# Performance work log

Measured on AMD Instinct MI355X. Metric: run time of the kernel, lower is better.

The kernel has to match this reference:

```python
import jax, jax.numpy as jnp
import numpy as np

N = 128                      # reduced state dimension (Q_dim[0])
S = N * (N + 1) // 2         # number of triu pairwise products = 8256
BATCH = 16384                # snapshot columns
_rows, _cols = np.triu_indices(N)
ROWS = jnp.asarray(_rows)    # [S] int32 constants
COLS = jnp.asarray(_cols)


def setup_inputs() -> dict:
    key = jax.random.key(0)
    kx, ka, kb = jax.random.split(key, 3)
    x = jax.random.normal(kx, (N, BATCH), dtype=jnp.float32)
    # learned operators (module inits them to zeros; use small random for a meaningful baseline)
    A = jax.random.normal(ka, (N, N), dtype=jnp.float32) * 0.02
    B = jax.random.normal(kb, (N, S), dtype=jnp.float32) * 0.02
    return {"x": x, "A": A, "B": B}


def reference(x, A, B):
    # quadratic feature expansion: x2[k, :] = x[i_k, :] * x[j_k, :] over triu pairs
    x2 = x[ROWS] * x[COLS]                 # [S, BATCH]
    return A @ x + B @ x2                  # [N, BATCH]
```

## Files before the change

### kernel.cpp

```cpp
#include <hip/hip_runtime.h>


constexpr int N_     = 128;
constexpr int S_     = 8256;
constexpr int BATCH_ = 16384;
constexpr int KTOT   = 8384;
constexpr int NKT    = 131;
constexpr size_t WT_BYTES = (size_t)KTOT * 128 * 2;
constexpr size_t PP_OFF   = WT_BYTES;
constexpr size_t XH_OFF   = PP_OFF + 32768;

typedef __attribute__((ext_vector_type(8))) _Float16 half8;
typedef __attribute__((ext_vector_type(2))) _Float16 half2t;
typedef __attribute__((ext_vector_type(4))) float f32x4;

typedef __attribute__((address_space(1))) const unsigned int gas_u32;
typedef __attribute__((address_space(3))) unsigned int las_u32;

__device__ __forceinline__ ushort f2h(float f) {
    _Float16 h = (_Float16)f;
    ushort b; __builtin_memcpy(&b, &h, 2); return b;
}
__device__ __forceinline__ float h2f(ushort b) {
    _Float16 h; __builtin_memcpy(&h, &b, 2); return (float)h;
}
__device__ __forceinline__ half2t duph(ushort b) {
    uint w = ((uint)b << 16) | (uint)b;
    half2t d; __builtin_memcpy(&d, &w, 4); return d;
}
__device__ __forceinline__ half8 mul_bc(half8 w, half2t d) {
    union { half8 h; half2t p[4]; } u, r;
    u.h = w;
    #pragma unroll
    for (int q = 0; q < 4; ++q) r.p[q] = u.p[q] * d;
    return r.h;
}

__device__ __forceinline__ int cumN(int i) {
    if (i <= 0) return 0;
    const int n = i - 1, t = n >> 3, r = n & 7;
    return 16 * i - (4 * t * (t + 1) + r * (t + 1));
}
__device__ __forceinline__ int offR(int i) {
    const int a = i >> 3, b = i & 7;
    const int p = b ? (8 * (b - 1) - (((b - 1) * b) >> 1)) : 0;
    return 28 * a + p;
}
__device__ __forceinline__ int triS(int i) { return i * (257 - i) / 2; }

__global__ __launch_bounds__(256) void build_all(
    const float* __restrict__ x,
    const float* __restrict__ A, const float* __restrict__ B,
    ushort* __restrict__ pp, ushort* __restrict__ wt,
    ushort* __restrict__ xh, float* __restrict__ out)
{
    const int bid = blockIdx.x, t = threadIdx.x;
    if (bid < 524) {
        const int idx = bid * 256 + t;
        const int ko  = idx >> 7;
        const int m   = idx & 127;
        const int kt = ko >> 3, kk = (ko >> 2) & 1, oct = ko & 3;
        const int lane = oct * 16 + (m & 15);
        const int e0 = kt * 8192 + kk * 4096 + (m >> 6) * 2048 +
                       ((m >> 4) & 3) * 512 + lane * 8;
        float v[8];
        if (ko < 16) {
            const int i0 = ko * 8;
            #pragma unroll
            for (int el = 0; el < 8; ++el) v[el] = A[m * 128 + i0 + el];
        } else if (ko < 992) {
            const int o = ko - 16;
            int i = 0;
            #pragma unroll
            for (int st = 64; st >= 1; st >>= 1) {
                const int c = i + st;
                if (c < 128 && cumN(c) <= o) i = c;
            }
            const int jb = ((i + 7) >> 3) + (o - cumN(i));
            const int s0 = triS(i) + jb * 8 - i;
            const float* bp = B + (size_t)m * S_ + s0;
            #pragma unroll
            for (int el = 0; el < 8; ++el) v[el] = bp[el];
        } else {
            const int kb = ko * 8 - 7936;
            #pragma unroll
            for (int el = 0; el < 8; ++el) {
                const int kloc = kb + el;
                int i = 0;
                #pragma unroll
                for (int st = 64; st >= 1; st >>= 1) {
                    const int c = i + st;
                    if (c < 128 && offR(c) <= kloc) i = c;
                }
                v[el] = B[(size_t)m * S_ + triS(i) + (kloc - offR(i))];
            }
        }
        ushort o8[8];
        #pragma unroll
        for (int el = 0; el < 8; ++el) o8[el] = f2h(v[el]);
        __builtin_memcpy(wt + e0, o8, 16);
    } else if (bid < 780) {
        const int zb = bid - 524;
        f32x4* o4 = (f32x4*)out;
        #pragma unroll
        for (int c = 0; c < 4; ++c)
            o4[(size_t)zb * 2048 + c * 512 + t] = (f32x4){0.f, 0.f, 0.f, 0.f};
    } else if (bid == 780) {
        const int i = t;
        if (i < 128) {
            pp[i] = (ushort)(i | (0xFFu << 8));
            const int jb0 = (i + 7) >> 3;
            int kb = 128 + cumN(i) * 8;
            for (int jb = jb0; jb < 16; ++jb) {
                #pragma unroll
                for (int e = 0; e < 8; ++e)
                    pp[kb + e] = (ushort)(i | ((jb * 8 + e) << 8));
                kb += 8;
            }
            const int h = (8 - (i & 7)) & 7;
            const int rb = 7936 + offR(i);
            for (int e = 0; e < h; ++e)
                pp[rb + e] = (ushort)(i | ((i + e) << 8));
        }
    } else {
        const int col = (bid - 781) * 256 + t;
        ushort* xc = xh + (size_t)col * 128;
        const int cs = col & 15;
        #pragma unroll
        for (int ro = 0; ro < 16; ++ro) {
            uint ow[4];
            #pragma unroll
            for (int p = 0; p < 4; ++p) {
                const ushort u0 = f2h(x[(size_t)(ro * 8 + 2 * p) * BATCH_ + col]);
                const ushort u1 = f2h(x[(size_t)(ro * 8 + 2 * p + 1) * BATCH_ + col]);
                ow[p] = (uint)u0 | ((uint)u1 << 16);
            }
            __builtin_memcpy(xc + ((ro ^ cs) << 3), ow, 16);
        }
    }
}

__device__ __forceinline__ void gload_lds16(const ushort* g, ushort* l) {
    __builtin_amdgcn_global_load_lds((gas_u32*)g, (las_u32*)l, 16, 0, 0);
}
__device__ __forceinline__ void stage_af(ushort* buf, const ushort* __restrict__ wt,
                                         int kt, int t) {
    const ushort* g = wt + ((size_t)kt << 13) + t * 8;
    gload_lds16(g, buf + t * 8);
    gload_lds16(g + 4096, buf + t * 8 + 4096);
}

__device__ __forceinline__ void load_af(half8 af[8], const ushort* __restrict__ wt,
                                        int kt, int wm, int lane) {
    const ushort* ab = wt + ((size_t)kt << 13) + (wm << 11) + (lane << 3);
    #pragma unroll
    for (int kk = 0; kk < 2; ++kk)
        #pragma unroll
        for (int mt = 0; mt < 4; ++mt)
            af[kk * 4 + mt] = *(const half8*)(ab + (kk << 12) + (mt << 9));
}

__device__ __forceinline__ void read_bin(ushort xi[2][4], half8 wj[2][4],
                                         uint prc,
                                         const ushort* __restrict__ xbase,
                                         int sw) {
    const int ia = (int)(prc & 0xFFu) ^ sw, ja = (int)((prc >> 8) & 0xFFu) ^ sw;
    const int ib = (int)((prc >> 16) & 0xFFu) ^ sw, jb = (int)(prc >> 24) ^ sw;
    #pragma unroll
    for (int nt = 0; nt < 4; ++nt) {
        const ushort* xb = xbase + nt * 2048;
        xi[0][nt] = xb[ia];
        xi[1][nt] = xb[ib];
        wj[0][nt] = *(const half8*)(xb + ja);
        wj[1][nt] = *(const half8*)(xb + jb);
    }
}

__device__ __forceinline__ void mfma_step(f32x4 acc[4][4], const half8 af[8],
                                          const ushort xi[2][4],
                                          const half8 wj[2][4]) {
    half8 bfr[2][4];
    #pragma unroll
    for (int kk = 0; kk < 2; ++kk)
        #pragma unroll
        for (int nt = 0; nt < 4; ++nt)
            bfr[kk][nt] = mul_bc(wj[kk][nt], duph(xi[kk][nt]));
    __builtin_amdgcn_s_setprio(1);
    #pragma unroll
    for (int kk = 0; kk < 2; ++kk)
        #pragma unroll
        for (int nt = 0; nt < 4; ++nt)
            #pragma unroll
            for (int mt = 0; mt < 4; ++mt)
                acc[mt][nt] = __builtin_amdgcn_mfma_f32_16x16x32_f16(
                    af[kk * 4 + mt], bfr[kk][nt], acc[mt][nt], 0, 0, 0);
    __builtin_amdgcn_s_setprio(0);
}

__global__ __launch_bounds__(512) void gemm_mfma(
    const ushort* __restrict__ xh,
    const ushort* __restrict__ wt,
    const ushort* __restrict__ pp,
    float* __restrict__ out)
{
    __shared__ ushort xt[256 * 128];
    __shared__ ushort afb[2][8192];
    __shared__ uint   ppc[NKT * 4];

    const int t    = threadIdx.x;
    const int b0   = blockIdx.x * 256;
    const int sp   = blockIdx.y;
    const int kt0  = sp * 33;
    const int kt1  = (sp == 3) ? NKT : kt0 + 33;
    const int lane = t & 63;
    const int w    = t >> 6;
    const int wm   = w >> 2, wn = w & 3;
    const int l16  = lane & 15, quad = lane >> 4;
    const int sw   = l16 << 3;

    const int s_ni = (kt0 > 2) ? kt0 : 2;
    const int e_ni = (kt1 < 124) ? kt1 : 124;

    {
        const ushort* src = xh + (size_t)b0 * 128;
        #pragma unroll
        for (int i = 0; i < 8; ++i)
            *(half8*)(xt + i * 4096 + t * 8) =
                *(const half8*)(src + i * 4096 + t * 8);
    }
    for (int idx = t; idx < NKT * 4; idx += 512) {
        const int kt = idx >> 2, q = idx & 3;
        const uint a0 = *(const uint*)(pp + kt * 64 + q * 8);
        const uint a1 = *(const uint*)(pp + kt * 64 + 32 + q * 8);
        ppc[idx] = (a0 & 0xFFFFu) | ((a1 & 0xFFFFu) << 16);
    }
    stage_af(&afb[0][0], wt, s_ni, t);

    f32x4 acc[4][4];
    #pragma unroll
    for (int mt = 0; mt < 4; ++mt)
        #pragma unroll
        for (int nt = 0; nt < 4; ++nt)
            acc[mt][nt] = (f32x4){0.f, 0.f, 0.f, 0.f};

    __syncthreads();

    const ushort* xbase = xt + (wn * 64 + l16) * 128;

    if (sp == 0) {
        for (int kt = 0; kt < 2; ++kt) {
            half8 af[8];
            load_af(af, wt, kt, wm, lane);
            #pragma unroll
            for (int kk = 0; kk < 2; ++kk) {
                const int off = (kt * 64 + kk * 32 + quad * 8) ^ sw;
                #pragma unroll
                for (int nt = 0; nt < 4; ++nt) {
                    const half8 bfr = *(const half8*)(xbase + nt * 2048 + off);
                    #pragma unroll
                    for (int mt = 0; mt < 4; ++mt)
                        acc[mt][nt] = __builtin_amdgcn_mfma_f32_16x16x32_f16(
                            af[kk * 4 + mt], bfr, acc[mt][nt], 0, 0, 0);
                }
            }
        }
    }

    {
        int cur = 0;
        uint prc = ppc[s_ni * 4 + quad];
        for (int kt = s_ni; kt < e_ni; ++kt) {
            if (kt > s_ni) {
                asm volatile("s_waitcnt vmcnt(0)" ::: "memory");
                __builtin_amdgcn_s_barrier();
                asm volatile("" ::: "memory");
            }
            if (kt + 1 < e_ni) stage_af(&afb[cur ^ 1][0], wt, kt + 1, t);
            const int ktn = (kt + 1 < e_ni) ? kt + 1 : kt;
            const uint prcN = ppc[ktn * 4 + quad];

            const ushort* ab = &afb[cur][0] + (wm << 11) + (lane << 3);
            half8 af[8];
            #pragma unroll
            for (int kk = 0; kk < 2; ++kk)
                #pragma unroll
                for (int mt = 0; mt < 4; ++mt)
                    af[kk * 4 + mt] = *(const half8*)(ab + (kk << 12) + (mt << 9));

            ushort xi[2][4]; half8 wj[2][4];
            read_bin(xi, wj, prc, xbase, sw);

            mfma_step(acc, af, xi, wj);

            prc = prcN;
            cur ^= 1;
        }
    }

    if (sp == 3) {
        for (int kt = 124; kt < NKT; ++kt) {
            half8 af[8];
            load_af(af, wt, kt, wm, lane);
            #pragma unroll
            for (int kk = 0; kk < 2; ++kk) {
                const int k0 = kt * 64 + kk * 32 + quad * 8;
                const uint4 pk = *(const uint4*)(pp + k0);
                const uint pr4[4] = {pk.x, pk.y, pk.z, pk.w};
                #pragma unroll
                for (int nt = 0; nt < 4; ++nt) {
                    const ushort* xb = xbase + nt * 2048;
                    float prods[8];
                    #pragma unroll
                    for (int e = 0; e < 8; ++e) {
                        const uint ent = (pr4[e >> 1] >> ((e & 1) * 16)) & 0xFFFFu;
                        prods[e] = h2f(xb[(int)(ent & 0xFFu) ^ sw]) *
                                   h2f(xb[(int)(ent >> 8) ^ sw]);
                    }
                    union { half8 h; uint wdw[4]; } bb;
                    #pragma unroll
                    for (int p = 0; p < 4; ++p) {
                        const auto pk2 = __builtin_amdgcn_cvt_pkrtz(
                            prods[2 * p], prods[2 * p + 1]);
                        __builtin_memcpy(&bb.wdw[p], &pk2, 4);
                    }
                    const half8 bfr = bb.h;
                    #pragma unroll
                    for (int mt = 0; mt < 4; ++mt)
                        acc[mt][nt] = __builtin_amdgcn_mfma_f32_16x16x32_f16(
                            af[kk * 4 + mt], bfr, acc[mt][nt], 0, 0, 0);
                }
            }
        }
    }

    #pragma unroll
    for (int mt = 0; mt < 4; ++mt) {
        #pragma unroll
        for (int nt = 0; nt < 4; ++nt) {
            const int mbase = wm * 64 + mt * 16 + quad * 4;
            const size_t col = (size_t)b0 + wn * 64 + nt * 16 + l16;
            #pragma unroll
            for (int r = 0; r < 4; ++r)
                unsafeAtomicAdd(&out[(size_t)(mbase + r) * BATCH_ + col],
                                acc[mt][nt][r]);
        }
    }
}

extern "C" void kernel_launch(void* const* d_in, const int* in_sizes, int n_in,
                              void* d_out, int out_size, void* d_ws, size_t ws_size,
                              hipStream_t stream) {
    const float* x = (const float*)d_in[0];
    const float* A = (const float*)d_in[1];
    const float* B = (const float*)d_in[2];
    float* out = (float*)d_out;

    ushort* wt = (ushort*)d_ws;
    ushort* pp = (ushort*)((char*)d_ws + PP_OFF);
    ushort* xh = (ushort*)((char*)d_ws + XH_OFF);

    build_all<<<845, 256, 0, stream>>>(x, A, B, pp, wt, xh, out);
    gemm_mfma<<<dim3(BATCH_ / 256, 4), 512, 0, stream>>>(xh, wt, pp, out);
}
```

Measured before the change: 129.5 us.

## Replace K-split with M-split and small tiles, drop atomics and output zeroing

The GEMM grid changes from 64 column-blocks × 4 K-splits with 256×128 tiles and atomic accumulation to 256 column-blocks × 2 M-halves with 64-column tiles. Each block now runs the full K range and writes its output directly, so the out-zeroing pass in the build kernel and the float atomics are gone. The LDS double-buffered async staging of weights is replaced by direct global loads per iteration. The cost is that each block reloads the full weight slice from global/L2 with no software prefetch, and the tiles are smaller, so each weight load is reused across fewer columns.

```diff
diff --git a/kernel.cpp b/kernel.cpp
--- a/kernel.cpp
+++ b/kernel.cpp
@@ -14,9 +14,6 @@
 typedef __attribute__((ext_vector_type(2))) _Float16 half2t;
 typedef __attribute__((ext_vector_type(4))) float f32x4;
 
-typedef __attribute__((address_space(1))) const unsigned int gas_u32;
-typedef __attribute__((address_space(3))) unsigned int las_u32;
-
 __device__ __forceinline__ ushort f2h(float f) {
     _Float16 h = (_Float16)f;
     ushort b; __builtin_memcpy(&b, &h, 2); return b;
@@ -52,7 +49,7 @@
     const float* __restrict__ x,
     const float* __restrict__ A, const float* __restrict__ B,
     ushort* __restrict__ pp, ushort* __restrict__ wt,
-    ushort* __restrict__ xh, float* __restrict__ out)
+    ushort* __restrict__ xh)
 {
     const int bid = blockIdx.x, t = threadIdx.x;
     if (bid < 524) {
@@ -99,13 +96,7 @@
         #pragma unroll
         for (int el = 0; el < 8; ++el) o8[el] = f2h(v[el]);
         __builtin_memcpy(wt + e0, o8, 16);
-    } else if (bid < 780) {
-        const int zb = bid - 524;
-        f32x4* o4 = (f32x4*)out;
-        #pragma unroll
-        for (int c = 0; c < 4; ++c)
-            o4[(size_t)zb * 2048 + c * 512 + t] = (f32x4){0.f, 0.f, 0.f, 0.f};
-    } else if (bid == 780) {
+    } else if (bid == 524) {
         const int i = t;
         if (i < 128) {
             pp[i] = (ushort)(i | (0xFFu << 8));
@@ -123,7 +114,7 @@
                 pp[rb + e] = (ushort)(i | ((i + e) << 8));
         }
     } else {
-        const int col = (bid - 781) * 256 + t;
+        const int col = (bid - 525) * 256 + t;
         ushort* xc = xh + (size_t)col * 128;
         const int cs = col & 15;
         #pragma unroll
@@ -140,209 +131,157 @@
     }
 }
 
-__device__ __forceinline__ void gload_lds16(const ushort* g, ushort* l) {
-    __builtin_amdgcn_global_load_lds((gas_u32*)g, (las_u32*)l, 16, 0, 0);
-}
-__device__ __forceinline__ void stage_af(ushort* buf, const ushort* __restrict__ wt,
-                                         int kt, int t) {
-    const ushort* g = wt + ((size_t)kt << 13) + t * 8;
-    gload_lds16(g, buf + t * 8);
-    gload_lds16(g + 4096, buf + t * 8 + 4096);
-}
-
-__device__ __forceinline__ void load_af(half8 af[8], const ushort* __restrict__ wt,
-                                        int kt, int wm, int lane) {
-    const ushort* ab = wt + ((size_t)kt << 13) + (wm << 11) + (lane << 3);
+__device__ __forceinline__ void load_af4(half8 af[4], const ushort* __restrict__ wt,
+                                         int kt, int mb, int wm, int lane) {
+    const ushort* ab = wt + ((size_t)kt << 13) + (mb << 11) + (wm << 10) +
+                       (lane << 3);
     #pragma unroll
     for (int kk = 0; kk < 2; ++kk)
         #pragma unroll
-        for (int mt = 0; mt < 4; ++mt)
-            af[kk * 4 + mt] = *(const half8*)(ab + (kk << 12) + (mt << 9));
-}
-
-__device__ __forceinline__ void read_bin(ushort xi[2][4], half8 wj[2][4],
-                                         uint prc,
-                                         const ushort* __restrict__ xbase,
-                                         int sw) {
-    const int ia = (int)(prc & 0xFFu) ^ sw, ja = (int)((prc >> 8) & 0xFFu) ^ sw;
-    const int ib = (int)((prc >> 16) & 0xFFu) ^ sw, jb = (int)(prc >> 24) ^ sw;
-    #pragma unroll
-    for (int nt = 0; nt < 4; ++nt) {
-        const ushort* xb = xbase + nt * 2048;
-        xi[0][nt] = xb[ia];
-        xi[1][nt] = xb[ib];
-        wj[0][nt] = *(const half8*)(xb + ja);
-        wj[1][nt] = *(const half8*)(xb + jb);
-    }
-}
-
-__device__ __forceinline__ void mfma_step(f32x4 acc[4][4], const half8 af[8],
-                                          const ushort xi[2][4],
-                                          const half8 wj[2][4]) {
-    half8 bfr[2][4];
-    #pragma unroll
-    for (int kk = 0; kk < 2; ++kk)
-        #pragma unroll
-        for (int nt = 0; nt < 4; ++nt)
-            bfr[kk][nt] = mul_bc(wj[kk][nt], duph(xi[kk][nt]));
-    __builtin_amdgcn_s_setprio(1);
-    #pragma unroll
-    for (int kk = 0; kk < 2; ++kk)
-        #pragma unroll
-        for (int nt = 0; nt < 4; ++nt)
-            #pragma unroll
-            for (int mt = 0; mt < 4; ++mt)
-                acc[mt][nt] = __builtin_amdgcn_mfma_f32_16x16x32_f16(
-                    af[kk * 4 + mt], bfr[kk][nt], acc[mt][nt], 0, 0, 0);
-    __builtin_amdgcn_s_setprio(0);
-}
-
-__global__ __launch_bounds__(512) void gemm_mfma(
+        for (int mt = 0; mt < 2; ++mt)
+            af[kk * 2 + mt] = *(const half8*)(ab + (kk << 12) + (mt << 9));
+}
+
+__global__ __launch_bounds__(256) void gemm_mfma(
     const ushort* __restrict__ xh,
     const ushort* __restrict__ wt,
     const ushort* __restrict__ pp,
     float* __restrict__ out)
 {
-    __shared__ ushort xt[256 * 128];
-    __shared__ ushort afb[2][8192];
+    __shared__ ushort xt[64 * 128];
     __shared__ uint   ppc[NKT * 4];
 
     const int t    = threadIdx.x;
-    const int b0   = blockIdx.x * 256;
-    const int sp   = blockIdx.y;
-    const int kt0  = sp * 33;
-    const int kt1  = (sp == 3) ? NKT : kt0 + 33;
+    const int b0   = blockIdx.x * 64;
+    const int mb   = blockIdx.y;
     const int lane = t & 63;
     const int w    = t >> 6;
-    const int wm   = w >> 2, wn = w & 3;
+    const int wm   = w >> 1, wn = w & 1;
     const int l16  = lane & 15, quad = lane >> 4;
     const int sw   = l16 << 3;
 
-    const int s_ni = (kt0 > 2) ? kt0 : 2;
-    const int e_ni = (kt1 < 124) ? kt1 : 124;
-
     {
         const ushort* src = xh + (size_t)b0 * 128;
         #pragma unroll
-        for (int i = 0; i < 8; ++i)
-            *(half8*)(xt + i * 4096 + t * 8) =
-                *(const half8*)(src + i * 4096 + t * 8);
-    }
-    for (int idx = t; idx < NKT * 4; idx += 512) {
+        for (int i = 0; i < 4; ++i)
+            *(half8*)(xt + i * 2048 + t * 8) =
+                *(const half8*)(src + i * 2048 + t * 8);
+    }
+    for (int idx = t; idx < NKT * 4; idx += 256) {
         const int kt = idx >> 2, q = idx & 3;
         const uint a0 = *(const uint*)(pp + kt * 64 + q * 8);
         const uint a1 = *(const uint*)(pp + kt * 64 + 32 + q * 8);
         ppc[idx] = (a0 & 0xFFFFu) | ((a1 & 0xFFFFu) << 16);
     }
-    stage_af(&afb[0][0], wt, s_ni, t);
-
-    f32x4 acc[4][4];
+    __syncthreads();
+
+    f32x4 acc[2][2];
     #pragma unroll
-    for (int mt = 0; mt < 4; ++mt)
-        #pragma unroll
-        for (int nt = 0; nt < 4; ++nt)
+    for (int mt = 0; mt < 2; ++mt)
+        #pragma unroll
+        for (int nt = 0; nt < 2; ++nt)
             acc[mt][nt] = (f32x4){0.f, 0.f, 0.f, 0.f};
 
-    __syncthreads();
-
-    const ushort* xbase = xt + (wn * 64 + l16) * 128;
-
-    if (sp == 0) {
-        for (int kt = 0; kt < 2; ++kt) {
-            half8 af[8];
-            load_af(af, wt, kt, wm, lane);
-            #pragma unroll
-            for (int kk = 0; kk < 2; ++kk) {
-                const int off = (kt * 64 + kk * 32 + quad * 8) ^ sw;
-                #pragma unroll
-                for (int nt = 0; nt < 4; ++nt) {
-                    const half8 bfr = *(const half8*)(xbase + nt * 2048 + off);
-                    #pragma unroll
-                    for (int mt = 0; mt < 4; ++mt)
-                        acc[mt][nt] = __builtin_amdgcn_mfma_f32_16x16x32_f16(
-                            af[kk * 4 + mt], bfr, acc[mt][nt], 0, 0, 0);
+    const ushort* xbase = xt + (wn * 32 + l16) * 128;
+
+    for (int kt = 0; kt < 2; ++kt) {
+        half8 af[4];
+        load_af4(af, wt, kt, mb, wm, lane);
+        #pragma unroll
+        for (int kk = 0; kk < 2; ++kk) {
+            const int off = (kt * 64 + kk * 32 + quad * 8) ^ sw;
+            #pragma unroll
+            for (int nt = 0; nt < 2; ++nt) {
+                const half8 bfr = *(const half8*)(xbase + nt * 2048 + off);
+                #pragma unroll
+                for (int mt = 0; mt < 2; ++mt)
+                    acc[mt][nt] = __builtin_amdgcn_mfma_f32_16x16x32_f16(
+                        af[kk * 2 + mt], bfr, acc[mt][nt], 0, 0, 0);
+            }
+        }
+    }
+
+    for (int kt = 2; kt < 124; ++kt) {
+        half8 af[4];
+        load_af4(af, wt, kt, mb, wm, lane);
+        const uint prc = ppc[kt * 4 + quad];
+        const int ia = (int)(prc & 0xFFu) ^ sw;
+        const int ja = (int)((prc >> 8) & 0xFFu) ^ sw;
+        const int ib = (int)((prc >> 16) & 0xFFu) ^ sw;
+        const int jb = (int)(prc >> 24) ^ sw;
+
+        ushort xi[2][2]; half8 wj[2][2];
+        #pragma unroll
+        for (int nt = 0; nt < 2; ++nt) {
+            const ushort* xb = xbase + nt * 2048;
+            xi[0][nt] = xb[ia];
+            xi[1][nt] = xb[ib];
+            wj[0][nt] = *(const half8*)(xb + ja);
+            wj[1][nt] = *(const half8*)(xb + jb);
+        }
+
+        half8 bfr[2][2];
+        #pragma unroll
+        for (int kk = 0; kk < 2; ++kk)
+            #pragma unroll
+            for (int nt = 0; nt < 2; ++nt)
+                bfr[kk][nt] = mul_bc(wj[kk][nt], duph(xi[kk][nt]));
+
+        __builtin_amdgcn_s_setprio(1);
+        #pragma unroll
+        for (int kk = 0; kk < 2; ++kk)
+            #pragma unroll
+            for (int nt = 0; nt < 2; ++nt)
+                #pragma unroll
+                for (int mt = 0; mt < 2; ++mt)
+                    acc[mt][nt] = __builtin_amdgcn_mfma_f32_16x16x32_f16(
+                        af[kk * 2 + mt], bfr[kk][nt], acc[mt][nt], 0, 0, 0);
+        __builtin_amdgcn_s_setprio(0);
+    }
+
+    for (int kt = 124; kt < NKT; ++kt) {
+        half8 af[4];
+        load_af4(af, wt, kt, mb, wm, lane);
+        #pragma unroll
+        for (int kk = 0; kk < 2; ++kk) {
+            const int k0 = kt * 64 + kk * 32 + quad * 8;
+            const uint4 pk = *(const uint4*)(pp + k0);
+            const uint pr4[4] = {pk.x, pk.y, pk.z, pk.w};
+            #pragma unroll
+            for (int nt = 0; nt < 2; ++nt) {
+                const ushort* xb = xbase + nt * 2048;
+                float prods[8];
+                #pragma unroll
+                for (int e = 0; e < 8; ++e) {
+                    const uint ent = (pr4[e >> 1] >> ((e & 1) * 16)) & 0xFFFFu;
+                    prods[e] = h2f(xb[(int)(ent & 0xFFu) ^ sw]) *
+                               h2f(xb[(int)(ent >> 8) ^ sw]);
                 }
-            }
-        }
-    }
-
-    {
-        int cur = 0;
-        uint prc = ppc[s_ni * 4 + quad];
-        for (int kt = s_ni; kt < e_ni; ++kt) {
-            if (kt > s_ni) {
-                asm volatile("s_waitcnt vmcnt(0)" ::: "memory");
-                __builtin_amdgcn_s_barrier();
-                asm volatile("" ::: "memory");
-            }
-            if (kt + 1 < e_ni) stage_af(&afb[cur ^ 1][0], wt, kt + 1, t);
-            const int ktn = (kt + 1 < e_ni) ? kt + 1 : kt;
-            const uint prcN = ppc[ktn * 4 + quad];
-
-            const ushort* ab = &afb[cur][0] + (wm << 11) + (lane << 3);
-            half8 af[8];
-            #pragma unroll
-            for (int kk = 0; kk < 2; ++kk)
-                #pragma unroll
-                for (int mt = 0; mt < 4; ++mt)
-                    af[kk * 4 + mt] = *(const half8*)(ab + (kk << 12) + (mt << 9));
-
-            ushort xi[2][4]; half8 wj[2][4];
-            read_bin(xi, wj, prc, xbase, sw);
-
-            mfma_step(acc, af, xi, wj);
-
-            prc = prcN;
-            cur ^= 1;
-        }
-    }
-
-    if (sp == 3) {
-        for (int kt = 124; kt < NKT; ++kt) {
-            half8 af[8];
-            load_af(af, wt, kt, wm, lane);
-            #pragma unroll
-            for (int kk = 0; kk < 2; ++kk) {
-                const int k0 = kt * 64 + kk * 32 + quad * 8;
-                const uint4 pk = *(const uint4*)(pp + k0);
-                const uint pr4[4] = {pk.x, pk.y, pk.z, pk.w};
-                #pragma unroll
-                for (int nt = 0; nt < 4; ++nt) {
-                    const ushort* xb = xbase + nt * 2048;
-                    float prods[8];
-                    #pragma unroll
-                    for (int e = 0; e < 8; ++e) {
-                        const uint ent = (pr4[e >> 1] >> ((e & 1) * 16)) & 0xFFFFu;
-                        prods[e] = h2f(xb[(int)(ent & 0xFFu) ^ sw]) *
-                                   h2f(xb[(int)(ent >> 8) ^ sw]);
-                    }
-                    union { half8 h; uint wdw[4]; } bb;
-                    #pragma unroll
-                    for (int p = 0; p < 4; ++p) {
-                        const auto pk2 = __builtin_amdgcn_cvt_pkrtz(
-                            prods[2 * p], prods[2 * p + 1]);
-                        __builtin_memcpy(&bb.wdw[p], &pk2, 4);
-                    }
-                    const half8 bfr = bb.h;
-                    #pragma unroll
-                    for (int mt = 0; mt < 4; ++mt)
-                        acc[mt][nt] = __builtin_amdgcn_mfma_f32_16x16x32_f16(
-                            af[kk * 4 + mt], bfr, acc[mt][nt], 0, 0, 0);
+                union { half8 h; uint wdw[4]; } bb;
+                #pragma unroll
+                for (int p = 0; p < 4; ++p) {
+                    const auto pk2 = __builtin_amdgcn_cvt_pkrtz(
+                        prods[2 * p], prods[2 * p + 1]);
+                    __builtin_memcpy(&bb.wdw[p], &pk2, 4);
                 }
+                const half8 bfr = bb.h;
+                #pragma unroll
+                for (int mt = 0; mt < 2; ++mt)
+                    acc[mt][nt] = __builtin_amdgcn_mfma_f32_16x16x32_f16(
+                        af[kk * 2 + mt], bfr, acc[mt][nt], 0, 0, 0);
             }
         }
     }
 
     #pragma unroll
-    for (int mt = 0; mt < 4; ++mt) {
-        #pragma unroll
-        for (int nt = 0; nt < 4; ++nt) {
-            const int mbase = wm * 64 + mt * 16 + quad * 4;
-            const size_t col = (size_t)b0 + wn * 64 + nt * 16 + l16;
+    for (int mt = 0; mt < 2; ++mt) {
+        #pragma unroll
+        for (int nt = 0; nt < 2; ++nt) {
+            const int mbase = mb * 64 + wm * 32 + mt * 16 + quad * 4;
+            const size_t col = (size_t)b0 + wn * 32 + nt * 16 + l16;
             #pragma unroll
             for (int r = 0; r < 4; ++r)
-                unsafeAtomicAdd(&out[(size_t)(mbase + r) * BATCH_ + col],
-                                acc[mt][nt][r]);
+                out[(size_t)(mbase + r) * BATCH_ + col] = acc[mt][nt][r];
         }
     }
 }
@@ -359,6 +298,6 @@
     ushort* pp = (ushort*)((char*)d_ws + PP_OFF);
     ushort* xh = (ushort*)((char*)d_ws + XH_OFF);
 
-    build_all<<<845, 256, 0, stream>>>(x, A, B, pp, wt, xh, out);
-    gemm_mfma<<<dim3(BATCH_ / 256, 4), 512, 0, stream>>>(xh, wt, pp, out);
-}
+    build_all<<<589, 256, 0, stream>>>(x, A, B, pp, wt, xh);
+    gemm_mfma<<<dim3(BATCH_ / 64, 2), 256, 0, stream>>>(xh, wt, pp, out);
+}
```

Result: no change. 130.8 us (+1.0%).
